# Optimization experiments

Measured on AMD Instinct MI355X. Metric: run time of the kernel, lower is better.

The kernel has to match this reference:

```python
import jax, jax.numpy as jnp
import numpy as np

K = 4096            # ca3_memory_slots
C = 2048            # ca3_code_dim
B = 8192            # query batch (episodes)
MAX_ITERS = 8       # cfg.pseudoinverse_iterations (spiking window T=8)
TOL = 1e-4          # cfg.convergence_tolerance
ALPHA_CLAMP = 5e-4  # torch.clamp(exp(log_scale), max=5e-4)


def setup_inputs() -> dict:
    key = jax.random.key(0)
    k1, k2, k3 = jax.random.split(key, 3)
    query = jax.random.normal(k1, (B, C), dtype=jnp.float32)
    # buffer init: torch.randn(K, C) * 0.01
    memory_mean = jax.random.normal(k2, (K, C), dtype=jnp.float32) * 0.01
    # nn.Parameter(torch.tensor(pseudoinverse_alpha_init)) -> scalar
    ben_israel_log_scale = jnp.float32(-0.5)
    return {"query": query, "memory_mean": memory_mean,
            "ben_israel_log_scale": ben_israel_log_scale}


def _ben_israel_pinv(A, log_scale):
    """Ben-Israel-Cohen iteration with masked early stopping (fixed trip count)."""
    A_fro_sq = jnp.sum(A * A)
    alpha = (1.0 / (A_fro_sq + 1e-8)) * jnp.minimum(jnp.exp(log_scale), ALPHA_CLAMP)
    pinv = alpha * A.T                       # (C, K)
    residual = jnp.array(jnp.inf, dtype=A.dtype)
    done = jnp.array(False)
    for _ in range(MAX_ITERS):
        pinv_new = 2.0 * pinv - pinv @ (A @ pinv)        # (C,K)
        recon = A @ (pinv_new @ A)                       # (K,C)
        res_new = jnp.linalg.norm(recon - A)             # Frobenius
        pinv = jnp.where(done, pinv, pinv_new)
        residual = jnp.where(done, residual, res_new)
        done = done | (res_new < TOL)
    return pinv, residual


def reference(query, memory_mean, ben_israel_log_scale):
    A = memory_mean                                      # (K, C)
    A_pinv, residual = _ben_israel_pinv(A, ben_israel_log_scale)  # (C, K)
    w = query @ A_pinv                                   # (B, K) addressing weights
    retrieved = w @ A                                    # (B, C) pattern completion
    return retrieved
```

## Files before the change

### kernel.cpp

```cpp
#include <hip/hip_runtime.h>
#include <hip/hip_bf16.h>
#include <cstdint>
#include <cstddef>


#define K_DIM 4096
#define C_DIM 2048
#define B_DIM 8192
#define SPLITK 4
#define KCHUNK (K_DIM / SPLITK)

typedef __bf16 bf16x8 __attribute__((ext_vector_type(8)));
typedef float f32x4 __attribute__((ext_vector_type(4)));

#define VMCNT(n) asm volatile("s_waitcnt vmcnt(" #n ")" ::: "memory")
#define LGKMCNT0 asm volatile("s_waitcnt lgkmcnt(0)" ::: "memory")
#define SBAR __builtin_amdgcn_s_barrier()

__device__ __forceinline__ void async_load16(const void* g, void* l) {
  __builtin_amdgcn_global_load_lds(
      (const __attribute__((address_space(1))) void*)g,
      (__attribute__((address_space(3))) void*)l, 16, 0, 0);
}

__global__ __launch_bounds__(256) void prep_kernel(
    const float* __restrict__ A, __hip_bfloat16* __restrict__ At,
    const float* __restrict__ q, __hip_bfloat16* __restrict__ qb,
    float* __restrict__ wsf) {
  const int b = blockIdx.x;
  const int t = threadIdx.x;
  if (b < 2048) {
    __shared__ __align__(16) __hip_bfloat16 Ts[64 * 68];
    const int c0 = (b & 31) * 64;
    const int k0 = (b >> 5) * 64;
    const int c_l = t & 63;
    const int kq = t >> 6;
#pragma unroll
    for (int i = 0; i < 4; ++i) {
      int k_l = i * 16 + kq * 4;
      union { __hip_bfloat16 h[4]; uint2 u; } pk;
#pragma unroll
      for (int j = 0; j < 4; ++j)
        pk.h[j] = __float2bfloat16(A[(size_t)(k0 + k_l + j) * C_DIM + c0 + c_l]);
      *(uint2*)(Ts + c_l * 68 + k_l) = pk.u;
    }
    __syncthreads();
    const int c = t >> 2;
    const int seg = t & 3;
    const __hip_bfloat16* src = Ts + c * 68 + seg * 16;
    union { uint2 d[2]; uint4 qv; } o0, o1;
    o0.d[0] = *(const uint2*)(src + 0);
    o0.d[1] = *(const uint2*)(src + 4);
    o1.d[0] = *(const uint2*)(src + 8);
    o1.d[1] = *(const uint2*)(src + 12);
    __hip_bfloat16* dst = At + (size_t)(c0 + c) * K_DIM + k0 + seg * 16;
    *(uint4*)(dst + 0) = o0.qv;
    *(uint4*)(dst + 8) = o1.qv;
  } else {
    if (b == 2048 && t == 0) wsf[4] = 0.0f;
    const int n4 = B_DIM * C_DIM / 4;
    int tid = (b - 2048) * 256 + t;
    for (int i = tid; i < n4; i += 1024 * 256) {
      float4 v = ((const float4*)q)[i];
      __hip_bfloat16 o[4] = {__float2bfloat16(v.x), __float2bfloat16(v.y),
                             __float2bfloat16(v.z), __float2bfloat16(v.w)};
      *(uint2*)(qb + 4 * (size_t)i) = *(const uint2*)o;
    }
  }
}

__global__ __launch_bounds__(256, 4) void gemm_m(
    const __hip_bfloat16* __restrict__ At, float* __restrict__ P) {
  constexpr int BK = 64;
  constexpr int NT = KCHUNK / BK;
  __shared__ __align__(16) __hip_bfloat16 As[128 * BK];
  __shared__ __align__(16) __hip_bfloat16 Bs[128 * BK];
  const int bid = blockIdx.x;
  const int sw = (bid & 7) * 128 + (bid >> 3);
  const int z = sw >> 8;
  const int r = sw & 255;
  const int tn_i = r >> 4;
  const int tm_i = r & 15;
  const int tid = threadIdx.x;
  const int wave = tid >> 6, lane = tid & 63;
  const int tile_m = tm_i * 128, tile_n = tn_i * 128;
  const int kstart = z * KCHUNK;
  const int wm = (wave >> 1) * 64, wn = (wave & 1) * 64;
  const int lr = lane >> 3, lcl = (lane & 7) ^ lr;
  const __hip_bfloat16* aB =
      At + (size_t)(tile_m + wave * 32 + lr) * K_DIM + kstart + lcl * 8;
  const __hip_bfloat16* bB =
      At + (size_t)(tile_n + wave * 32 + lr) * K_DIM + kstart + lcl * 8;
  const int l15 = lane & 15, lg = lane >> 4, l7 = lane & 7;
  f32x4 acc[4][4] = {};

  for (int t = 0; t < NT; ++t) {
#pragma unroll
    for (int c = 0; c < 4; ++c) {
      async_load16(aB + (size_t)(c * 8) * K_DIM + (size_t)t * BK,
                   &As[(wave * 32 + c * 8) * BK]);
      async_load16(bB + (size_t)(c * 8) * K_DIM + (size_t)t * BK,
                   &Bs[(wave * 32 + c * 8) * BK]);
    }
    __syncthreads();
#pragma unroll
    for (int kh = 0; kh < 2; ++kh) {
      bf16x8 a[4], bb[4];
#pragma unroll
      for (int f = 0; f < 4; ++f) {
        a[f]  = *(const bf16x8*)&As[(wm + f * 16 + l15) * BK +
                                    (((kh * 4 + lg) ^ l7) * 8)];
        bb[f] = *(const bf16x8*)&Bs[(wn + f * 16 + l15) * BK +
                                    (((kh * 4 + lg) ^ l7) * 8)];
      }
      __builtin_amdgcn_s_setprio(1);
#pragma unroll
      for (int f = 0; f < 4; ++f)
#pragma unroll
        for (int j = 0; j < 4; ++j)
          acc[f][j] = __builtin_amdgcn_mfma_f32_16x16x32_bf16(
              a[f], bb[j], acc[f][j], 0, 0, 0);
      __builtin_amdgcn_s_setprio(0);
    }
    __syncthreads();
  }

  float* Pz = P + (size_t)z * C_DIM * C_DIM;
#pragma unroll
  for (int f = 0; f < 4; ++f) {
    const int gm = tile_m + wm + f * 16 + lg * 4;
#pragma unroll
    for (int j = 0; j < 4; ++j) {
      const int gn = tile_n + wn + j * 16 + l15;
#pragma unroll
      for (int r2 = 0; r2 < 4; ++r2)
        Pz[(size_t)(gm + r2) * C_DIM + gn] = acc[f][j][r2];
    }
  }
}

__global__ __launch_bounds__(256) void reduce4_kernel(
    const float* __restrict__ P, __hip_bfloat16* __restrict__ Mb,
    float* __restrict__ wsf) {
  const size_t CC = (size_t)C_DIM * C_DIM;
  const int n4 = (int)(CC / 4);
  int tid = blockIdx.x * blockDim.x + threadIdx.x;
  int stride = gridDim.x * blockDim.x;
  float tsum = 0.0f;
  bool hit = false;
  for (int i = tid; i < n4; i += stride) {
    float4 a = ((const float4*)P)[i];
#pragma unroll
    for (int z = 1; z < SPLITK; ++z) {
      float4 b = *(const float4*)(P + z * CC + (size_t)i * 4);
      a.x += b.x; a.y += b.y; a.z += b.z; a.w += b.w;
    }
    __hip_bfloat16 o[4] = {__float2bfloat16(a.x), __float2bfloat16(a.y),
                           __float2bfloat16(a.z), __float2bfloat16(a.w)};
    *(uint2*)(Mb + 4 * (size_t)i) = *(const uint2*)o;
    const int e0 = 4 * i;
    const int g = e0 >> 11;
    const int d = g * (C_DIM + 1);
    if (d >= e0 && d < e0 + 4) {
      const float av[4] = {a.x, a.y, a.z, a.w};
      tsum += av[d - e0];
      hit = true;
    }
  }
  if (hit) atomicAdd(wsf + 4, tsum);
}

__global__ __launch_bounds__(512, 2) void gemm_qm(
    const __hip_bfloat16* __restrict__ Ab, const __hip_bfloat16* __restrict__ Bb,
    float* __restrict__ Fp, const float* __restrict__ ls,
    const float* __restrict__ wsf) {
  constexpr int BK = 64;
  constexpr int NT = C_DIM / BK;
  __shared__ __align__(16) __hip_bfloat16 As[2][256 * BK];
  __shared__ __align__(16) __hip_bfloat16 Bs[2][256 * BK];
  const int bid = blockIdx.x;
  const int sw = (bid & 7) * 32 + (bid >> 3);
  const int tn_i = sw & 7;
  const int tm_i = sw >> 3;
  const int tid = threadIdx.x;
  const int wave = tid >> 6, lane = tid & 63;
  const int tile_m = tm_i * 256, tile_n = tn_i * 256;
  const int wm = (wave >> 2) * 128, wn = (wave & 3) * 64;
  const int lr = lane >> 3, lcl = (lane & 7) ^ lr;
  const __hip_bfloat16* aBase =
      Ab + (size_t)(tile_m + wave * 16 + lr) * C_DIM + lcl * 8;
  const __hip_bfloat16* bBase =
      Bb + (size_t)(tile_n + wave * 16 + lr) * C_DIM + lcl * 8;
  const int l15 = lane & 15, lg = lane >> 4, l7 = lane & 7;

  auto stA = [&](int buf, int h, int t) {
    const __hip_bfloat16* s = aBase + (size_t)(h * 128) * C_DIM + (size_t)t * BK;
    __hip_bfloat16* d = &As[buf][(h * 128 + wave * 16) * BK];
    async_load16(s, d);
    async_load16(s + (size_t)8 * C_DIM, d + 8 * BK);
  };
  auto stB = [&](int buf, int h, int t) {
    const __hip_bfloat16* s = bBase + (size_t)(h * 128) * C_DIM + (size_t)t * BK;
    __hip_bfloat16* d = &Bs[buf][(h * 128 + wave * 16) * BK];
    async_load16(s, d);
    async_load16(s + (size_t)8 * C_DIM, d + 8 * BK);
  };

  f32x4 acc[8][4] = {};

  stA(0, 0, 0); stA(0, 1, 0);
  stB(0, 0, 0); stB(0, 1, 0);
  stB(1, 0, 1); stB(1, 1, 1);
  VMCNT(4);
  SBAR;

  for (int t = 0; t < NT; ++t) {
    const int buf = t & 1;
    bf16x8 breg[4][2];
#pragma unroll
    for (int q = 0; q < 4; ++q) {
      bf16x8 af[2][2];
#pragma unroll
      for (int f = 0; f < 2; ++f)
#pragma unroll
        for (int s = 0; s < 2; ++s)
          af[f][s] = *(const bf16x8*)&As[buf][(wm + q * 32 + f * 16 + l15) * BK +
                                             ((((s << 2) | lg) ^ l7) << 3)];
      if (q == 0) {
#pragma unroll
        for (int j = 0; j < 4; ++j)
#pragma unroll
          for (int s = 0; s < 2; ++s)
            breg[j][s] = *(const bf16x8*)&Bs[buf][(wn + j * 16 + l15) * BK +
                                                 ((((s << 2) | lg) ^ l7) << 3)];
      }
      if (q == 0 && t + 1 < NT) stA(buf ^ 1, 0, t + 1);
      if (q == 1 && t + 1 < NT) stA(buf ^ 1, 1, t + 1);
      if (q == 2 && t + 2 < NT) stB(buf, 0, t + 2);
      if (q == 3) {
        if (t + 2 < NT) {
          stB(buf, 1, t + 2);
          VMCNT(4);
        } else {
          VMCNT(0);
        }
      }
      SBAR;
      LGKMCNT0;
      __builtin_amdgcn_s_setprio(1);
#pragma unroll
      for (int s = 0; s < 2; ++s)
#pragma unroll
        for (int f = 0; f < 2; ++f)
#pragma unroll
          for (int j = 0; j < 4; ++j)
            acc[q * 2 + f][j] = __builtin_amdgcn_mfma_f32_16x16x32_bf16(
                af[f][s], breg[j][s], acc[q * 2 + f][j], 0, 0, 0);
      __builtin_amdgcn_s_setprio(0);
      SBAR;
    }
  }

  const float c1 = 256.0f * fminf(expf(ls[0]), 5e-4f) / (wsf[4] + 1e-8f);
#pragma unroll
  for (int m = 0; m < 8; ++m) {
    const int gm = tile_m + wm + m * 16 + lg * 4;
#pragma unroll
    for (int j = 0; j < 4; ++j) {
      const int gn = tile_n + wn + j * 16 + l15;
#pragma unroll
      for (int r = 0; r < 4; ++r)
        Fp[(size_t)(gm + r) * C_DIM + gn] = c1 * acc[m][j][r];
    }
  }
}

extern "C" void kernel_launch(void* const* d_in, const int* in_sizes, int n_in,
                              void* d_out, int out_size, void* d_ws, size_t ws_size,
                              hipStream_t stream) {
  const float* query = (const float*)d_in[0];
  const float* A = (const float*)d_in[1];
  const float* ls = (const float*)d_in[2];
  float* out = (float*)d_out;

  char* ws = (char*)d_ws;
  float* wsf = (float*)ws;
  size_t off = 256;
  __hip_bfloat16* At = (__hip_bfloat16*)(ws + off);
  off += (size_t)C_DIM * K_DIM * 2;
  __hip_bfloat16* qb = (__hip_bfloat16*)(ws + off);
  off += (size_t)B_DIM * C_DIM * 2;
  __hip_bfloat16* Mb = (__hip_bfloat16*)(ws + off);

  float* P = out;

  prep_kernel<<<3072, 256, 0, stream>>>(A, At, query, qb, wsf);
  gemm_m<<<1024, 256, 0, stream>>>(At, P);
  reduce4_kernel<<<1024, 256, 0, stream>>>(P, Mb, wsf);
  gemm_qm<<<256, 512, 0, stream>>>(qb, Mb, out, ls, wsf);
}
```

Measured before the change: 275.3 us.

## Enlarge split-K Gram GEMM tiles, store bf16 partials, restructure qm pipeline

The A^T A split-K GEMM moves from 128x128 single-buffered tiles to 256x256 double-buffered tiles with 512 threads, reusing the pipelined scheme from the second GEMM. Its partial sums are now written as bf16 rather than fp32, which halves the partial-buffer write and reduce-read traffic at some cost in accumulation precision. The second GEMM's inner loop is rescheduled to read operands once per half-K slab and issue 16 MFMAs per barrier, with fewer barriers per tile. That reschedule also changes when the async loads are waited on.

```diff
diff --git a/kernel.cpp b/kernel.cpp
--- a/kernel.cpp
+++ b/kernel.cpp
@@ -69,101 +69,139 @@
   }
 }
 
-__global__ __launch_bounds__(256, 4) void gemm_m(
-    const __hip_bfloat16* __restrict__ At, float* __restrict__ P) {
+__global__ __launch_bounds__(512, 2) void gemm_m3(
+    const __hip_bfloat16* __restrict__ At, __hip_bfloat16* __restrict__ P) {
   constexpr int BK = 64;
   constexpr int NT = KCHUNK / BK;
-  __shared__ __align__(16) __hip_bfloat16 As[128 * BK];
-  __shared__ __align__(16) __hip_bfloat16 Bs[128 * BK];
+  __shared__ __align__(16) __hip_bfloat16 As[2][256 * BK];
+  __shared__ __align__(16) __hip_bfloat16 Bs[2][256 * BK];
   const int bid = blockIdx.x;
-  const int sw = (bid & 7) * 128 + (bid >> 3);
-  const int z = sw >> 8;
-  const int r = sw & 255;
-  const int tn_i = r >> 4;
-  const int tm_i = r & 15;
+  const int sw = (bid & 7) * 32 + (bid >> 3);
+  const int z = sw >> 6;
+  const int rem = sw & 63;
+  const int tm_i = rem >> 3;
+  const int tn_i = rem & 7;
   const int tid = threadIdx.x;
   const int wave = tid >> 6, lane = tid & 63;
-  const int tile_m = tm_i * 128, tile_n = tn_i * 128;
+  const int tile_m = tm_i * 256, tile_n = tn_i * 256;
   const int kstart = z * KCHUNK;
-  const int wm = (wave >> 1) * 64, wn = (wave & 1) * 64;
+  const int wm = (wave >> 2) * 128, wn = (wave & 3) * 64;
   const int lr = lane >> 3, lcl = (lane & 7) ^ lr;
-  const __hip_bfloat16* aB =
-      At + (size_t)(tile_m + wave * 32 + lr) * K_DIM + kstart + lcl * 8;
-  const __hip_bfloat16* bB =
-      At + (size_t)(tile_n + wave * 32 + lr) * K_DIM + kstart + lcl * 8;
+  const __hip_bfloat16* aBase =
+      At + (size_t)(tile_m + wave * 16 + lr) * K_DIM + kstart + lcl * 8;
+  const __hip_bfloat16* bBase =
+      At + (size_t)(tile_n + wave * 16 + lr) * K_DIM + kstart + lcl * 8;
   const int l15 = lane & 15, lg = lane >> 4, l7 = lane & 7;
-  f32x4 acc[4][4] = {};
+
+  auto stA = [&](int buf, int h, int t) {
+    const __hip_bfloat16* s = aBase + (size_t)(h * 128) * K_DIM + (size_t)t * BK;
+    __hip_bfloat16* d = &As[buf][(h * 128 + wave * 16) * BK];
+    async_load16(s, d);
+    async_load16(s + (size_t)8 * K_DIM, d + 8 * BK);
+  };
+  auto stB = [&](int buf, int h, int t) {
+    const __hip_bfloat16* s = bBase + (size_t)(h * 128) * K_DIM + (size_t)t * BK;
+    __hip_bfloat16* d = &Bs[buf][(h * 128 + wave * 16) * BK];
+    async_load16(s, d);
+    async_load16(s + (size_t)8 * K_DIM, d + 8 * BK);
+  };
+
+  f32x4 acc[8][4] = {};
+
+  stA(0, 0, 0); stA(0, 1, 0);
+  stB(0, 0, 0); stB(0, 1, 0);
+  stB(1, 0, 1); stB(1, 1, 1);
+  VMCNT(4);
+  SBAR;
 
   for (int t = 0; t < NT; ++t) {
-#pragma unroll
-    for (int c = 0; c < 4; ++c) {
-      async_load16(aB + (size_t)(c * 8) * K_DIM + (size_t)t * BK,
-                   &As[(wave * 32 + c * 8) * BK]);
-      async_load16(bB + (size_t)(c * 8) * K_DIM + (size_t)t * BK,
-                   &Bs[(wave * 32 + c * 8) * BK]);
-    }
-    __syncthreads();
-#pragma unroll
-    for (int kh = 0; kh < 2; ++kh) {
-      bf16x8 a[4], bb[4];
-#pragma unroll
-      for (int f = 0; f < 4; ++f) {
-        a[f]  = *(const bf16x8*)&As[(wm + f * 16 + l15) * BK +
-                                    (((kh * 4 + lg) ^ l7) * 8)];
-        bb[f] = *(const bf16x8*)&Bs[(wn + f * 16 + l15) * BK +
-                                    (((kh * 4 + lg) ^ l7) * 8)];
+    const int buf = t & 1;
+    bf16x8 breg[4][2];
+#pragma unroll
+    for (int q = 0; q < 4; ++q) {
+      bf16x8 af[2][2];
+#pragma unroll
+      for (int f = 0; f < 2; ++f)
+#pragma unroll
+        for (int s = 0; s < 2; ++s)
+          af[f][s] = *(const bf16x8*)&As[buf][(wm + q * 32 + f * 16 + l15) * BK +
+                                             ((((s << 2) | lg) ^ l7) << 3)];
+      if (q == 0) {
+#pragma unroll
+        for (int j = 0; j < 4; ++j)
+#pragma unroll
+          for (int s = 0; s < 2; ++s)
+            breg[j][s] = *(const bf16x8*)&Bs[buf][(wn + j * 16 + l15) * BK +
+                                                 ((((s << 2) | lg) ^ l7) << 3)];
       }
+      if (q == 0 && t + 1 < NT) stA(buf ^ 1, 0, t + 1);
+      if (q == 1 && t + 1 < NT) stA(buf ^ 1, 1, t + 1);
+      if (q == 2 && t + 2 < NT) stB(buf, 0, t + 2);
+      if (q == 3) {
+        if (t + 2 < NT) {
+          stB(buf, 1, t + 2);
+          VMCNT(4);
+        } else {
+          VMCNT(0);
+        }
+      }
+      SBAR;
+      LGKMCNT0;
       __builtin_amdgcn_s_setprio(1);
 #pragma unroll
-      for (int f = 0; f < 4; ++f)
-#pragma unroll
-        for (int j = 0; j < 4; ++j)
-          acc[f][j] = __builtin_amdgcn_mfma_f32_16x16x32_bf16(
-              a[f], bb[j], acc[f][j], 0, 0, 0);
+      for (int s = 0; s < 2; ++s)
+#pragma unroll
+        for (int f = 0; f < 2; ++f)
+#pragma unroll
+          for (int j = 0; j < 4; ++j)
+            acc[q * 2 + f][j] = __builtin_amdgcn_mfma_f32_16x16x32_bf16(
+                af[f][s], breg[j][s], acc[q * 2 + f][j], 0, 0, 0);
       __builtin_amdgcn_s_setprio(0);
-    }
-    __syncthreads();
-  }
-
-  float* Pz = P + (size_t)z * C_DIM * C_DIM;
-#pragma unroll
-  for (int f = 0; f < 4; ++f) {
-    const int gm = tile_m + wm + f * 16 + lg * 4;
+      SBAR;
+    }
+  }
+
+  __hip_bfloat16* Pz = P + (size_t)z * C_DIM * C_DIM;
+#pragma unroll
+  for (int m = 0; m < 8; ++m) {
+    const int gm = tile_m + wm + m * 16 + lg * 4;
 #pragma unroll
     for (int j = 0; j < 4; ++j) {
       const int gn = tile_n + wn + j * 16 + l15;
 #pragma unroll
-      for (int r2 = 0; r2 < 4; ++r2)
-        Pz[(size_t)(gm + r2) * C_DIM + gn] = acc[f][j][r2];
+      for (int r = 0; r < 4; ++r)
+        Pz[(size_t)(gm + r) * C_DIM + gn] = __float2bfloat16(acc[m][j][r]);
     }
   }
 }
 
 __global__ __launch_bounds__(256) void reduce4_kernel(
-    const float* __restrict__ P, __hip_bfloat16* __restrict__ Mb,
+    const __hip_bfloat16* __restrict__ P, __hip_bfloat16* __restrict__ Mb,
     float* __restrict__ wsf) {
   const size_t CC = (size_t)C_DIM * C_DIM;
-  const int n4 = (int)(CC / 4);
+  const int n8 = (int)(CC / 8);
   int tid = blockIdx.x * blockDim.x + threadIdx.x;
   int stride = gridDim.x * blockDim.x;
   float tsum = 0.0f;
   bool hit = false;
-  for (int i = tid; i < n4; i += stride) {
-    float4 a = ((const float4*)P)[i];
-#pragma unroll
-    for (int z = 1; z < SPLITK; ++z) {
-      float4 b = *(const float4*)(P + z * CC + (size_t)i * 4);
-      a.x += b.x; a.y += b.y; a.z += b.z; a.w += b.w;
-    }
-    __hip_bfloat16 o[4] = {__float2bfloat16(a.x), __float2bfloat16(a.y),
-                           __float2bfloat16(a.z), __float2bfloat16(a.w)};
-    *(uint2*)(Mb + 4 * (size_t)i) = *(const uint2*)o;
-    const int e0 = 4 * i;
+  for (int i = tid; i < n8; i += stride) {
+    float acc[8] = {};
+#pragma unroll
+    for (int z = 0; z < SPLITK; ++z) {
+      uint4 raw = *(const uint4*)(P + z * CC + (size_t)i * 8);
+      const __hip_bfloat16* h = (const __hip_bfloat16*)&raw;
+#pragma unroll
+      for (int j = 0; j < 8; ++j) acc[j] += __bfloat162float(h[j]);
+    }
+    __hip_bfloat16 o[8];
+#pragma unroll
+    for (int j = 0; j < 8; ++j) o[j] = __float2bfloat16(acc[j]);
+    *(uint4*)(Mb + (size_t)i * 8) = *(const uint4*)o;
+    const int e0 = 8 * i;
     const int g = e0 >> 11;
     const int d = g * (C_DIM + 1);
-    if (d >= e0 && d < e0 + 4) {
-      const float av[4] = {a.x, a.y, a.z, a.w};
-      tsum += av[d - e0];
+    if (d >= e0 && d < e0 + 8) {
+      tsum += acc[d - e0];
       hit = true;
     }
   }
@@ -207,6 +245,30 @@
   };
 
   f32x4 acc[8][4] = {};
+  bf16x8 af[4], bfr[4];
+
+  auto rdA = [&](int buf, int mh, int s) {
+#pragma unroll
+    for (int f = 0; f < 4; ++f)
+      af[f] = *(const bf16x8*)&As[buf][(wm + mh * 64 + f * 16 + l15) * BK +
+                                       (((s * 4 + lg) ^ l7) * 8)];
+  };
+  auto rdB = [&](int buf, int s) {
+#pragma unroll
+    for (int j = 0; j < 4; ++j)
+      bfr[j] = *(const bf16x8*)&Bs[buf][(wn + j * 16 + l15) * BK +
+                                        (((s * 4 + lg) ^ l7) * 8)];
+  };
+  auto mm = [&](int mh) {
+    __builtin_amdgcn_s_setprio(1);
+#pragma unroll
+    for (int f = 0; f < 4; ++f)
+#pragma unroll
+      for (int j = 0; j < 4; ++j)
+        acc[mh * 4 + f][j] = __builtin_amdgcn_mfma_f32_16x16x32_bf16(
+            af[f], bfr[j], acc[mh * 4 + f][j], 0, 0, 0);
+    __builtin_amdgcn_s_setprio(0);
+  };
 
   stA(0, 0, 0); stA(0, 1, 0);
   stB(0, 0, 0); stB(0, 1, 0);
@@ -216,49 +278,28 @@
 
   for (int t = 0; t < NT; ++t) {
     const int buf = t & 1;
-    bf16x8 breg[4][2];
-#pragma unroll
-    for (int q = 0; q < 4; ++q) {
-      bf16x8 af[2][2];
-#pragma unroll
-      for (int f = 0; f < 2; ++f)
-#pragma unroll
-        for (int s = 0; s < 2; ++s)
-          af[f][s] = *(const bf16x8*)&As[buf][(wm + q * 32 + f * 16 + l15) * BK +
-                                             ((((s << 2) | lg) ^ l7) << 3)];
-      if (q == 0) {
-#pragma unroll
-        for (int j = 0; j < 4; ++j)
-#pragma unroll
-          for (int s = 0; s < 2; ++s)
-            breg[j][s] = *(const bf16x8*)&Bs[buf][(wn + j * 16 + l15) * BK +
-                                                 ((((s << 2) | lg) ^ l7) << 3)];
-      }
-      if (q == 0 && t + 1 < NT) stA(buf ^ 1, 0, t + 1);
-      if (q == 1 && t + 1 < NT) stA(buf ^ 1, 1, t + 1);
-      if (q == 2 && t + 2 < NT) stB(buf, 0, t + 2);
-      if (q == 3) {
-        if (t + 2 < NT) {
-          stB(buf, 1, t + 2);
-          VMCNT(4);
-        } else {
-          VMCNT(0);
-        }
-      }
-      SBAR;
-      LGKMCNT0;
-      __builtin_amdgcn_s_setprio(1);
-#pragma unroll
-      for (int s = 0; s < 2; ++s)
-#pragma unroll
-        for (int f = 0; f < 2; ++f)
-#pragma unroll
-          for (int j = 0; j < 4; ++j)
-            acc[q * 2 + f][j] = __builtin_amdgcn_mfma_f32_16x16x32_bf16(
-                af[f][s], breg[j][s], acc[q * 2 + f][j], 0, 0, 0);
-      __builtin_amdgcn_s_setprio(0);
-      SBAR;
-    }
+    rdA(buf, 0, 0);
+    rdB(buf, 0);
+    SBAR;
+    if (t + 1 < NT) stA(buf ^ 1, 0, t + 1);
+    LGKMCNT0;
+    mm(0);
+    rdA(buf, 1, 0);
+    SBAR;
+    if (t + 1 < NT) stA(buf ^ 1, 1, t + 1);
+    LGKMCNT0;
+    mm(1);
+    rdA(buf, 0, 1);
+    rdB(buf, 1);
+    SBAR;
+    LGKMCNT0;
+    mm(0);
+    rdA(buf, 1, 1);
+    VMCNT(0);
+    SBAR;
+    if (t + 2 < NT) { stB(buf, 0, t + 2); stB(buf, 1, t + 2); }
+    LGKMCNT0;
+    mm(1);
   }
 
   const float c1 = 256.0f * fminf(expf(ls[0]), 5e-4f) / (wsf[4] + 1e-8f);
@@ -292,10 +333,10 @@
   off += (size_t)B_DIM * C_DIM * 2;
   __hip_bfloat16* Mb = (__hip_bfloat16*)(ws + off);
 
-  float* P = out;
+  __hip_bfloat16* P = (__hip_bfloat16*)out;
 
   prep_kernel<<<3072, 256, 0, stream>>>(A, At, query, qb, wsf);
-  gemm_m<<<1024, 256, 0, stream>>>(At, P);
+  gemm_m3<<<256, 512, 0, stream>>>(At, P);
   reduce4_kernel<<<1024, 256, 0, stream>>>(P, Mb, wsf);
   gemm_qm<<<256, 512, 0, stream>>>(qb, Mb, out, ls, wsf);
 }
```

Result: no change. 276.8 us (+0.5%).
